# Kernel tuning notes

Hardware: AMD Instinct MI355X
Metric: run time of the kernel (lower is better)

The kernel has to match this reference:

```python
import jax, jax.numpy as jnp
import numpy as np

MAX_REL = 7  # maxRelativeDist

def _rel_pos_table(L, max_rel):
    # |i-j|, with distances beyond max_rel mapped to max_rel + log2(d - max_rel), clipped to [0, 2*max_rel]
    idx = jnp.arange(L)
    d = jnp.abs(idx[:, None] - idx[None, :]).astype(jnp.float32)
    far = d > max_rel
    d = jnp.where(far, max_rel + jnp.log2(jnp.maximum(d - max_rel, 1.0)), d)
    return jnp.clip(d, 0, 2 * max_rel).astype(jnp.int32)  # [L, L]

def setup_inputs() -> dict:
    key = jax.random.key(0)
    ks = jax.random.split(key, 16)
    B, L, C, P, H, DK = 8, 2048, 512, 64, 8, 64
    s = 0.02
    inp = {
        'qx': jax.random.normal(ks[0], (B, L, C), jnp.float32),
        'kx': jax.random.normal(ks[1], (B, L, C), jnp.float32),
        'vx': jax.random.normal(ks[2], (B, L, C), jnp.float32),
        'maskPAD': jnp.ones((B, L, L), jnp.int32),
        # pseudoAttn: Linear(C, P)
        'Wp': jax.random.normal(ks[3], (C, P), jnp.float32) * s,
        'bp': jnp.zeros((P,), jnp.float32),
        # WQ/WK: Linear(C, dkEnhance*DK*H) with dkEnhance=1
        'Wq': jax.random.normal(ks[4], (C, H * DK), jnp.float32) * s,
        'bq': jnp.zeros((H * DK,), jnp.float32),
        'Wk': jax.random.normal(ks[5], (C, H * DK), jnp.float32) * s,
        'bk': jnp.zeros((H * DK,), jnp.float32),
        'Wv': jax.random.normal(ks[6], (C, H * DK), jnp.float32) * s,
        'bv': jnp.zeros((H * DK,), jnp.float32),
        'Wo': jax.random.normal(ks[7], (H * DK, C), jnp.float32) * s,
        'bo': jnp.zeros((C,), jnp.float32),
        # relative position embeddings: [2*MAX_REL+1, H]
        'embK': jax.random.normal(ks[8], (2 * MAX_REL + 1, H), jnp.float32) * s,
        'embB': jax.random.normal(ks[9], (2 * MAX_REL + 1, H), jnp.float32) * s,
    }
    return inp

def reference(qx, kx, vx, maskPAD, Wp, bp, Wq, bq, Wk, bk, Wv, bv, Wo, bo, embK, embB):
    # dropout is identity (eval mode); preScores=None
    B, L, C = qx.shape
    H = embK.shape[1]
    DK = Wv.shape[1] // H
    P = Wp.shape[1]

    # pseudo-token compression
    pScore = vx @ Wp + bp                                   # [B, L, P]
    mask = (maskPAD[:, 0] == 0)[:, :, None]                 # [B, L, 1]
    pScore = jnp.where(mask, jnp.float32(-2.0 ** 15), pScore)
    pAlpha = jax.nn.softmax(pScore, axis=1)                 # softmax over L
    kxc = jnp.einsum('blp,blc->bpc', pAlpha, kx)            # [B, P, C]
    vxc = jnp.einsum('blp,blc->bpc', pAlpha, vx)            # [B, P, C]
    pAlpha_d = jax.lax.stop_gradient(pAlpha)

    # multi-head projections
    q = (qx @ Wq + bq).reshape(B, L, H, DK)                 # [B, L, H, DK]
    k = (kxc @ Wk + bk).reshape(B, P, H, DK)
    v = (vxc @ Wv + bv).reshape(B, P, H, DK)

    scores = jnp.einsum('blhd,bphd->bhlp', q, k) / np.sqrt(DK)  # [B, H, L, P]

    # relative-position modulation
    relTab = _rel_pos_table(L, MAX_REL)                     # [L, L] int
    Kmat = jnp.transpose(embK[relTab], (2, 1, 0))           # [H, L, L]
    Bmat = jnp.transpose(embB[relTab], (2, 1, 0))           # [H, L, L]
    Kterm = jnp.einsum('hlm,bmp->bhlp', Kmat, pAlpha_d)
    Bterm = jnp.einsum('hlm,bmp->bhlp', Bmat, pAlpha_d)
    scores = scores * Kterm + Bterm

    alpha = jax.nn.softmax(scores, axis=3)                  # over pseudo tokens
    z = jnp.einsum('bhlp,bphd->blhd', alpha, v).reshape(B, L, H * DK)
    z = z @ Wo + bo                                         # [B, L, C]
    return z, pScore, scores
```

## Files before the change

kernel.cpp:

```cpp
#include <hip/hip_runtime.h>


typedef __attribute__((ext_vector_type(8))) short bhalf8;
typedef __attribute__((ext_vector_type(4))) float fx4;

__device__ __forceinline__ unsigned short f2bf(float f) {
  union { float f; unsigned u; } v; v.f = f;
  unsigned u = v.u + 0x7fffu + ((v.u >> 16) & 1u);
  return (unsigned short)(u >> 16);
}
__device__ __forceinline__ float bf2f(unsigned short h) {
  union { unsigned u; float f; } v; v.u = ((unsigned)h) << 16;
  return v.f;
}
__device__ __forceinline__ void gld16(const void* g, void* l) {
  __builtin_amdgcn_global_load_lds(
      (const __attribute__((address_space(1))) void*)g,
      (__attribute__((address_space(3))) void*)l, 16, 0, 0);
}

template <int BM, int BN, int CMODE, int AF32, int KSPLIT, int BF32>
__device__ __forceinline__ void gemm_body(
    int bxx, int byy, int bzz, char* smemc,
    const void* __restrict__ Av, const unsigned short* __restrict__ BT,
    const float* __restrict__ bias, void* __restrict__ Cout,
    int K, int lda, int ldbt, int ldc, int HDIV,
    long sAb, long sAh, long sBb, long sBh, long sCb, long sCh, long sCk,
    const int* __restrict__ mpad, float* __restrict__ aux,
    const float* __restrict__ Bf32)
{
  constexpr int NA = BM / 16, NB = BN / 16, NT = NA + NB;
  constexpr int WM = BM / 2, WN = BN / 2, FM = WM / 16, FN = WN / 16;
  unsigned short* lds = (unsigned short*)smemc;
  const int t = threadIdx.x, l = t & 63, w = t >> 6;
  const int wr = w >> 1, wc = w & 1;
  const int zz = bzz, b = zz / HDIV, h = zz % HDIV;
  const int row0 = KSPLIT ? 0 : byy * BM;
  const int koff = KSPLIT ? byy * K : 0;
  const long cko = KSPLIT ? (long)byy * sCk : 0;
  const int col0 = bxx * BN;
  const unsigned short* Ag = (const unsigned short*)Av + b * sAb + h * sAh + (long)row0 * lda + koff;
  const float* AgF = (const float*)Av + b * sAb + h * sAh + (long)row0 * lda + koff;
  const unsigned short* Bg = BT + b * sBb + h * sBh + (long)col0 * ldbt + koff;
  const int lr = l & 15, lc = l >> 4;

  fx4 acc[FM][FN];
#pragma unroll
  for (int i = 0; i < FM; ++i)
#pragma unroll
    for (int j = 0; j < FN; ++j) acc[i][j] = fx4{0.f, 0.f, 0.f, 0.f};

  for (int k0 = 0; k0 < K; k0 += 32) {
#pragma unroll
    for (int i = 0; i < NT / 4; ++i) {
      const int tile = w + i * 4;
      bool handled = false;
      if constexpr (AF32 == 1) {
        if (tile < NA) {
          const float* gf = AgF + (long)(tile * 16 + lr) * lda + k0 + lc * 8;
          float4 x = *(const float4*)gf, y = *(const float4*)(gf + 4);
          bhalf8 pk;
          pk[0] = (short)f2bf(x.x); pk[1] = (short)f2bf(x.y);
          pk[2] = (short)f2bf(x.z); pk[3] = (short)f2bf(x.w);
          pk[4] = (short)f2bf(y.x); pk[5] = (short)f2bf(y.y);
          pk[6] = (short)f2bf(y.z); pk[7] = (short)f2bf(y.w);
          *(bhalf8*)&lds[tile * 512 + l * 8] = pk;
          handled = true;
        }
      } else if constexpr (AF32 == 2) {
        if (tile < NA) {
          const float* gf = (const float*)Av + (long)zz * sAb + (long)byy * 131072
                            + (long)(tile * 16 + lr) * 512 + k0 + lc * 8;
          float4 x = make_float4(0.f, 0.f, 0.f, 0.f), y = x;
#pragma unroll
          for (int c = 0; c < 4; ++c) {
            float4 a = *(const float4*)(gf + (long)c * 32768);
            float4 bq = *(const float4*)(gf + (long)c * 32768 + 4);
            x.x += a.x; x.y += a.y; x.z += a.z; x.w += a.w;
            y.x += bq.x; y.y += bq.y; y.z += bq.z; y.w += bq.w;
          }
          bhalf8 pk;
          pk[0] = (short)f2bf(x.x); pk[1] = (short)f2bf(x.y);
          pk[2] = (short)f2bf(x.z); pk[3] = (short)f2bf(x.w);
          pk[4] = (short)f2bf(y.x); pk[5] = (short)f2bf(y.y);
          pk[6] = (short)f2bf(y.z); pk[7] = (short)f2bf(y.w);
          *(bhalf8*)&lds[tile * 512 + l * 8] = pk;
          handled = true;
        }
      }
      if (!handled) {
        if constexpr (BF32 == 1) {
          const int ct = tile - NA;
          const float* gfB = Bf32 + (long)(k0 + lc * 8) * ldbt + col0 + ct * 16 + lr;
          bhalf8 pk;
#pragma unroll
          for (int i2 = 0; i2 < 8; ++i2) pk[i2] = (short)f2bf(gfB[(long)i2 * ldbt]);
          *(bhalf8*)&lds[tile * 512 + l * 8] = pk;
        } else {
          const unsigned short* g = (tile < NA)
              ? Ag + (long)(tile * 16 + lr) * lda + k0 + lc * 8
              : Bg + (long)((tile - NA) * 16 + lr) * ldbt + k0 + lc * 8;
          gld16(g, &lds[tile * 512]);
        }
      }
    }
    __syncthreads();
    bhalf8 af[FM], bf[FN];
#pragma unroll
    for (int i = 0; i < FM; ++i) af[i] = *(const bhalf8*)&lds[(wr * FM + i) * 512 + l * 8];
#pragma unroll
    for (int j = 0; j < FN; ++j) bf[j] = *(const bhalf8*)&lds[(NA + wc * FN + j) * 512 + l * 8];
#pragma unroll
    for (int i = 0; i < FM; ++i)
#pragma unroll
      for (int j = 0; j < FN; ++j)
        acc[i][j] = __builtin_amdgcn_mfma_f32_16x16x32_bf16(af[i], bf[j], acc[i][j], 0, 0, 0);
    __syncthreads();
  }

  if constexpr (CMODE == 3) {
    float (*tbuf)[65] = (float(*)[65])(smemc + NT * 1024);
#pragma unroll
    for (int fm = 0; fm < FM; ++fm) {
#pragma unroll
      for (int fn = 0; fn < FN; ++fn) {
        const int rg0 = row0 + wr * WM + fm * 16 + lc * 4;
        const int cg = col0 + wc * WN + fn * 16 + lr;
        const float bb = bias[cg];
#pragma unroll
        for (int jj = 0; jj < 4; ++jj) {
          const int rg = rg0 + jj;
          float vv = acc[fm][fn][jj] + bb;
          if (mpad[((long)(rg >> 11)) * (2048L * 2048) + (rg & 2047)] == 0) vv = -32768.f;
          __builtin_nontemporal_store(vv, (float*)Cout + (long)rg * ldc + cg);
          tbuf[rg - row0][cg] = vv;
        }
      }
    }
    __syncthreads();
    const int b0 = row0 >> 11, l0b = row0 & 2047;
    const int pp = t >> 2, li0 = (t & 3) * 16;
    float* dst = aux + ((long)b0 * 64 + pp) * 2048 + l0b + li0;
#pragma unroll
    for (int i = 0; i < 16; i += 4) {
      float4 o = make_float4(tbuf[li0 + i][pp],     tbuf[li0 + i + 1][pp],
                             tbuf[li0 + i + 2][pp], tbuf[li0 + i + 3][pp]);
      *(float4*)(dst + i) = o;
    }
  } else {
#pragma unroll
    for (int fm = 0; fm < FM; ++fm) {
#pragma unroll
      for (int fn = 0; fn < FN; ++fn) {
        const int rg0 = row0 + wr * WM + fm * 16 + lc * 4;
        const int cg = col0 + wc * WN + fn * 16 + lr;
        float bb = 0.f;
        if constexpr (CMODE == 4) {
          bb = (zz == 0) ? bias[cg] : ((const float*)mpad)[cg];
        } else {
          bb = bias ? bias[cg] : 0.f;
        }
#pragma unroll
        for (int jj = 0; jj < 4; ++jj) {
          const int rg = rg0 + jj;
          const float v = acc[fm][fn][jj] + bb;
          if constexpr (CMODE == 0) {
            ((float*)Cout)[b * sCb + h * sCh + cko + (long)rg * ldc + cg] = v;
          } else if constexpr (CMODE == 1) {
            ((unsigned short*)Cout)[b * sCb + h * sCh + (long)rg * ldc + cg] = f2bf(v);
          } else if constexpr (CMODE == 2) {
            ((unsigned short*)Cout)[(((long)(rg >> 6) * 8 + (cg >> 6)) * 64 + (cg & 63)) * 64 + (rg & 63)] = f2bf(v);
          } else if constexpr (CMODE == 4) {
            if (zz == 0)
              ((unsigned short*)Cout)[(long)rg * ldc + cg] = f2bf(v);
            else
              ((unsigned short*)Cout)[262144 + (((long)(rg >> 6) * 8 + (cg >> 6)) * 64 + (cg & 63)) * 64 + (rg & 63)] = f2bf(v);
          } else {
            __builtin_nontemporal_store(v, (float*)Cout + b * sCb + h * sCh + cko + (long)rg * ldc + cg);
          }
        }
      }
    }
  }
}

template <int BM, int BN, int CMODE, int AF32, int KSPLIT>
__global__ __launch_bounds__(256)
void gemm_mfma(const void* __restrict__ Av, const unsigned short* __restrict__ BT,
               const float* __restrict__ bias, void* __restrict__ Cout,
               int K, int lda, int ldbt, int ldc, int HDIV,
               long sAb, long sAh, long sBb, long sBh, long sCb, long sCh, long sCk,
               const int* __restrict__ mpad, float* __restrict__ aux)
{
  constexpr int SM = (BM / 16 + BN / 16) * 1024 + (CMODE == 3 ? 16640 : 0);
  __shared__ __align__(16) char smem[SM];
  gemm_body<BM, BN, CMODE, AF32, KSPLIT, 0>(blockIdx.x, blockIdx.y, blockIdx.z, smem,
      Av, BT, bias, Cout, K, lda, ldbt, ldc, HDIV,
      sAb, sAh, sBb, sBh, sCb, sCh, sCk, mpad, aux, nullptr);
}

__device__ __forceinline__ void tr_body(float (*tile)[65], const float* __restrict__ in,
                                        unsigned short* __restrict__ out,
                                        int R, int Cd, int r0, int c0, int t)
{
  const int tr = t >> 4, tc4 = (t & 15) * 4;
#pragma unroll
  for (int pass = 0; pass < 4; ++pass) {
    int r = pass * 16 + tr;
    float4 v = *(const float4*)(in + (long)(r0 + r) * Cd + c0 + tc4);
    tile[r][tc4] = v.x; tile[r][tc4 + 1] = v.y; tile[r][tc4 + 2] = v.z; tile[r][tc4 + 3] = v.w;
  }
  __syncthreads();
#pragma unroll
  for (int pass = 0; pass < 4; ++pass) {
    int c = pass * 16 + tr;
    ushort4 o;
    o.x = f2bf(tile[tc4][c]);     o.y = f2bf(tile[tc4 + 1][c]);
    o.z = f2bf(tile[tc4 + 2][c]); o.w = f2bf(tile[tc4 + 3][c]);
    *(ushort4*)(out + (long)(c0 + c) * R + r0 + tc4) = o;
  }
}

__global__ __launch_bounds__(256)
void combo0(const float* __restrict__ vx, const float* __restrict__ Wp,
            const float* __restrict__ bp, const int* __restrict__ maskPAD,
            float* __restrict__ ps_out, float* __restrict__ pScoreT,
            const float* __restrict__ kx,
            const float* __restrict__ Wq, const float* __restrict__ Wk,
            const float* __restrict__ Wv, const float* __restrict__ Wo,
            unsigned short* __restrict__ kxT, unsigned short* __restrict__ vxT,
            unsigned short* __restrict__ WqT, unsigned short* __restrict__ WkT,
            unsigned short* __restrict__ WvT, unsigned short* __restrict__ WoT)
{
  __shared__ __align__(16) char smem[24832];
  const int id = blockIdx.x;
  const long LC = 2048L * 512;
  if (id < 256) {
    gemm_body<64, 64, 3, 1, 0, 1>(0, id, 0, smem,
        vx, nullptr, bp, ps_out, 512, 512, 64, 64, 1,
        0, 0, 0, 0, 0, 0, 0, maskPAD, pScoreT, Wp);
  } else if (id < 4352) {
    const int r = id - 256;
    const int zz = r >> 8, rem = r & 255;
    const float* in = (zz < 8) ? kx + zz * LC : vx + (zz - 8) * LC;
    unsigned short* out = (zz < 8) ? kxT + zz * LC : vxT + (zz - 8) * LC;
    tr_body((float(*)[65])smem, in, out, 2048, 512, (rem >> 3) * 64, (rem & 7) * 64, threadIdx.x);
  } else if (id < 4608) {
    const int r = id - 4352;
    const int z = r >> 6, rem = r & 63;
    const float* in; unsigned short* out;
    switch (z) {
      case 0: in = Wq; out = WqT; break;
      case 1: in = Wk; out = WkT; break;
      case 2: in = Wv; out = WvT; break;
      default: in = Wo; out = WoT; break;
    }
    tr_body((float(*)[65])smem, in, out, 512, 512, (rem >> 3) * 64, (rem & 7) * 64, threadIdx.x);
  }
}

__device__ __forceinline__ void kb_body(int bx, int by, char* smemc,
    const unsigned short* __restrict__ PSb,
    const float* __restrict__ embK, const float* __restrict__ embB,
    ushort2* __restrict__ KB)
{
  const int L = 2048, STR = 338;
  unsigned short* psw = (unsigned short*)smemc;
  float (*eKs)[8] = (float(*)[8])(smemc + 43264);
  float (*eBs)[8] = (float(*)[8])(smemc + 43264 + 512);
  const int t = threadIdx.x, b = by, l0 = bx * 64;
  if (t < 128) {
    int r = t >> 3, h = t & 7;
    eKs[r][h] = (r < 15) ? embK[r * 8 + h] : 0.f;
    eBs[r][h] = (r < 15) ? embB[r * 8 + h] : 0.f;
  }
  const int W0 = l0 - 136;
  const int w = t >> 6, ln = t & 63;
  for (int pr = w * 16; pr < w * 16 + 16; ++pr) {
    const unsigned short* src = PSb + ((long)b * 64 + pr) * 2048;
#pragma unroll
    for (int pass = 0; pass < 6; ++pass) {
      int j = pass * 64 + ln;
      if (j < 337) {
        int g = (j == 336) ? (L - 1) : (W0 + j);
        g = g < 0 ? 0 : (g > L - 1 ? L - 1 : g);
        psw[pr * STR + j] = src[g];
      }
    }
  }
  __syncthreads();
  const int p = ln;
  const int Btab[14] = {0,1,2,3,4,5,6,8,10,14,22,38,70,134};
  for (int step = 0; step < 16; ++step) {
    const int l = l0 + w * 16 + step;
    float U[15];
#pragma unroll
    for (int r = 0; r < 14; ++r) {
      int hi = l + Btab[r]; hi = hi > L - 1 ? L - 1 : hi;
      float u = bf2f(psw[p * STR + (hi - W0)]);
      const int lo = l - 1 - Btab[r];
      if (lo >= 0) u -= bf2f(psw[p * STR + (lo - W0)]);
      U[r] = u;
    }
    U[14] = bf2f(psw[p * STR + 336]);
    for (int h = 0; h < 8; ++h) {
      float Kt = 0.f, Bt = 0.f;
#pragma unroll
      for (int r = 0; r < 15; ++r) {
        Kt = fmaf(eKs[r][h] - eKs[r + 1][h], U[r], Kt);
        Bt = fmaf(eBs[r][h] - eBs[r + 1][h], U[r], Bt);
      }
      ushort2 o; o.x = f2bf(Kt); o.y = f2bf(Bt);
      KB[(((long)(b * 8 + h)) * L + l) * 64 + p] = o;
    }
  }
}

__global__ __launch_bounds__(256)
void combo1(const unsigned short* __restrict__ pAbf, const unsigned short* __restrict__ kxT,
            float* __restrict__ pbuf,
            const unsigned short* __restrict__ PSb,
            const float* __restrict__ embK, const float* __restrict__ embB,
            ushort2* __restrict__ KB)
{
  __shared__ __align__(16) char smem[44544];
  const int id = blockIdx.x;
  if (id < 512) {
    gemm_body<64, 64, 0, 0, 1, 0>(id & 7, (id >> 3) & 3, id >> 5, smem,
        pAbf, kxT, nullptr, pbuf, 512, 2048, 2048, 512, 2,
        131072, 0, 1048576, 8388608, 131072, 1048576, 32768, nullptr, nullptr, nullptr);
  } else {
    const int r = id - 512;
    kb_body(r & 31, r >> 5, smem, PSb, embK, embB, KB);
  }
}

__global__ __launch_bounds__(256)
void combo2(const float* __restrict__ pbuf, const unsigned short* __restrict__ WkT,
            const float* __restrict__ bk, const float* __restrict__ bv,
            unsigned short* __restrict__ kp,
            const float* __restrict__ qx, const unsigned short* __restrict__ WqT,
            const float* __restrict__ bq, unsigned short* __restrict__ qbf)
{
  __shared__ __align__(16) char smem[16384];
  const int id = blockIdx.x;
  if (id < 64) {
    gemm_body<64, 128, 4, 2, 0, 0>(id & 3, (id >> 2) & 7, id >> 5, smem,
        pbuf, WkT, bk, kp, 512, 512, 512, 512, 1,
        1048576, 0, 262144, 0, 0, 0, 0, (const int*)bv, nullptr, nullptr);
  } else {
    const int r = id - 64;
    gemm_body<128, 128, 1, 1, 0, 0>(r & 3, r >> 2, 0, smem,
        qx, WqT, bq, qbf, 512, 512, 512, 512, 1,
        0, 0, 0, 0, 0, 0, 0, nullptr, nullptr, nullptr);
  }
}

__global__ __launch_bounds__(256)
void softmax_scan(const float* __restrict__ pScoreT,
                  unsigned short* __restrict__ PSb, unsigned short* __restrict__ pA_bf)
{
  __shared__ float red[256];
  const int p = blockIdx.x, b = blockIdx.y, t = threadIdx.x;
  const float* row = pScoreT + ((size_t)b * 64 + p) * 2048;
  float4 va = ((const float4*)row)[t * 2], vb = ((const float4*)row)[t * 2 + 1];
  float v[8] = {va.x, va.y, va.z, va.w, vb.x, vb.y, vb.z, vb.w};
  float mx = v[0];
#pragma unroll
  for (int i = 1; i < 8; ++i) mx = fmaxf(mx, v[i]);
  red[t] = mx; __syncthreads();
  for (int s = 128; s > 0; s >>= 1) { if (t < s) red[t] = fmaxf(red[t], red[t + s]); __syncthreads(); }
  float m = red[0]; __syncthreads();
  float e[8]; float s = 0.f;
#pragma unroll
  for (int i = 0; i < 8; ++i) { e[i] = expf(v[i] - m); s += e[i]; }
  red[t] = s; __syncthreads();
  for (int o = 1; o < 256; o <<= 1) {
    float x = (t >= o) ? red[t - o] : 0.f;
    __syncthreads(); red[t] += x; __syncthreads();
  }
  float inv = 1.0f / red[255];
  float run = red[t] - s;
  size_t base = ((size_t)b * 64 + p) * 2048 + (size_t)t * 8;
#pragma unroll
  for (int i = 0; i < 8; ++i) {
    run += e[i];
    PSb[base + i] = f2bf(run * inv);
    pA_bf[base + i] = f2bf(e[i] * inv);
  }
}

__global__ __launch_bounds__(256)
void attn_fused(const unsigned short* __restrict__ qb,
                const unsigned short* __restrict__ kp,
                const unsigned short* __restrict__ vpT,
                const ushort2* __restrict__ KB,
                float* __restrict__ sc_out,
                unsigned short* __restrict__ zpre)
{
  const int L = 2048;
  __shared__ __align__(16) unsigned short stg[24 * 512];
  unsigned short* qkb = &stg[8 * 512];
  const int t = threadIdx.x, l = t & 63, w = t >> 6, lr = l & 15, lc = l >> 4;
  const int flat = blockIdx.y * 16 + blockIdx.x;
  const int swz = (flat & 7) * 128 + (flat >> 3);
  const int z = swz >> 4, b = z >> 3, h = z & 7;
  const int l0 = (swz & 15) * 128;
  const unsigned short* Ag = qb + ((long)(b * L + l0)) * 512 + h * 64;
  const unsigned short* Bg = kp + (long)b * 64 * 512 + h * 64;
#pragma unroll
  for (int i = 0; i < 6; ++i) {
    const int tile = w + i * 4;
    const unsigned short* g;
    if (tile < 16) { int rt = tile >> 1, ks = tile & 1; g = Ag + (long)(rt * 16 + lr) * 512 + ks * 32 + lc * 8; }
    else { int j = tile - 16; int rt = j >> 1, ks = j & 1; g = Bg + (long)(rt * 16 + lr) * 512 + ks * 32 + lc * 8; }
    gld16(g, &stg[tile * 512]);
  }
  const ushort2* kbb = KB + (((long)(b * 8 + h)) * L + l0) * 64 + l;
  unsigned int kbreg[32];
#pragma unroll
  for (int i = 0; i < 32; ++i)
    kbreg[i] = *(const unsigned int*)(kbb + ((long)(w * 32 + i)) * 64);
  __syncthreads();
  const int wr = w >> 1, wc = w & 1;
  fx4 acc[4][2];
#pragma unroll
  for (int i = 0; i < 4; ++i)
#pragma unroll
    for (int j = 0; j < 2; ++j) acc[i][j] = fx4{0.f, 0.f, 0.f, 0.f};
#pragma unroll
  for (int ks = 0; ks < 2; ++ks) {
    bhalf8 af[4], bf[2];
#pragma unroll
    for (int i = 0; i < 4; ++i) af[i] = *(const bhalf8*)&stg[((wr * 4 + i) * 2 + ks) * 512 + l * 8];
#pragma unroll
    for (int j = 0; j < 2; ++j) bf[j] = *(const bhalf8*)&stg[(16 + (wc * 2 + j) * 2 + ks) * 512 + l * 8];
#pragma unroll
    for (int i = 0; i < 4; ++i)
#pragma unroll
      for (int j = 0; j < 2; ++j)
        acc[i][j] = __builtin_amdgcn_mfma_f32_16x16x32_bf16(af[i], bf[j], acc[i][j], 0, 0, 0);
  }
  __syncthreads();
#pragma unroll
  for (int fm = 0; fm < 4; ++fm)
#pragma unroll
    for (int fn = 0; fn < 2; ++fn)
#pragma unroll
      for (int jj = 0; jj < 4; ++jj) {
        const int row = wr * 64 + fm * 16 + lc * 4 + jj;
        const int col = wc * 32 + fn * 16 + lr;
        *(unsigned short*)((char*)qkb + ((row * 128 + col * 2) ^ ((row & 7) << 4))) = f2bf(acc[fm][fn][jj]);
      }
  __syncthreads();
  {
    const unsigned short* Vg = vpT + ((long)(b * 8 + h)) * 64 * 64;
#pragma unroll
    for (int i = 0; i < 2; ++i) {
      const int tile = w + i * 4, rt = tile >> 1, ks = tile & 1;
      gld16(Vg + (long)(rt * 16 + lr) * 64 + ks * 32 + lc * 8, &stg[tile * 512]);
    }
  }
  const int p = l;
  float* scb = sc_out + ((long)(b * 8 + h) * L + l0) * 64 + p;
#pragma unroll
  for (int c = 0; c < 8; ++c) {
    const int rbase = w * 32 + c * 4;
    float sv[4];
#pragma unroll
    for (int il = 0; il < 4; ++il) {
      const int row = rbase + il;
      const unsigned int kbw = kbreg[c * 4 + il];
      const float qkv = bf2f(*(const unsigned short*)((const char*)qkb + ((row * 128 + p * 2) ^ ((row & 7) << 4))));
      sv[il] = qkv * 0.125f * bf2f((unsigned short)(kbw & 0xffffu)) + bf2f((unsigned short)(kbw >> 16));
      __builtin_nontemporal_store(sv[il], scb + (long)row * 64);
    }
    float mx[4] = {sv[0], sv[1], sv[2], sv[3]};
#pragma unroll
    for (int o = 32; o > 0; o >>= 1)
#pragma unroll
      for (int il = 0; il < 4; ++il) mx[il] = fmaxf(mx[il], __shfl_xor(mx[il], o, 64));
    float ex[4], sm[4];
#pragma unroll
    for (int il = 0; il < 4; ++il) { ex[il] = __expf(sv[il] - mx[il]); sm[il] = ex[il]; }
#pragma unroll
    for (int o = 32; o > 0; o >>= 1)
#pragma unroll
      for (int il = 0; il < 4; ++il) sm[il] += __shfl_xor(sm[il], o, 64);
#pragma unroll
    for (int il = 0; il < 4; ++il) {
      const int row = rbase + il;
      *(unsigned short*)((char*)qkb + ((row * 128 + p * 2) ^ ((row & 7) << 4))) = f2bf(ex[il] / sm[il]);
    }
  }
  __syncthreads();
  fx4 a2[4][2];
#pragma unroll
  for (int i = 0; i < 4; ++i)
#pragma unroll
    for (int j = 0; j < 2; ++j) a2[i][j] = fx4{0.f, 0.f, 0.f, 0.f};
#pragma unroll
  for (int ks = 0; ks < 2; ++ks) {
    bhalf8 paf[4], pvf[2];
#pragma unroll
    for (int i = 0; i < 4; ++i) {
      const int row = (wr * 4 + i) * 16 + lr;
      paf[i] = *(const bhalf8*)((const char*)qkb + ((row * 128 + ks * 64 + lc * 16) ^ ((row & 7) << 4)));
    }
#pragma unroll
    for (int j = 0; j < 2; ++j)
      pvf[j] = *(const bhalf8*)&stg[(((wc * 2 + j) * 2 + ks) * 512) + l * 8];
#pragma unroll
    for (int i = 0; i < 4; ++i)
#pragma unroll
      for (int j = 0; j < 2; ++j)
        a2[i][j] = __builtin_amdgcn_mfma_f32_16x16x32_bf16(paf[i], pvf[j], a2[i][j], 0, 0, 0);
  }
#pragma unroll
  for (int fm = 0; fm < 4; ++fm)
#pragma unroll
    for (int fn = 0; fn < 2; ++fn)
#pragma unroll
      for (int jj = 0; jj < 4; ++jj) {
        const int row = wr * 64 + fm * 16 + lc * 4 + jj;
        const int col = wc * 32 + fn * 16 + lr;
        zpre[((long)(b * L + l0 + row)) * 512 + h * 64 + col] = f2bf(a2[fm][fn][jj]);
      }
}

extern "C" void kernel_launch(void* const* d_in, const int* in_sizes, int n_in,
                              void* d_out, int out_size, void* d_ws, size_t ws_size,
                              hipStream_t stream)
{
  const int B = 8, L = 2048, C = 512, P = 64;
  const float* qx = (const float*)d_in[0];
  const float* kx = (const float*)d_in[1];
  const float* vx = (const float*)d_in[2];
  const int* maskPAD = (const int*)d_in[3];
  const float* Wp = (const float*)d_in[4];
  const float* bp = (const float*)d_in[5];
  const float* Wq = (const float*)d_in[6];
  const float* bq = (const float*)d_in[7];
  const float* Wk = (const float*)d_in[8];
  const float* bk = (const float*)d_in[9];
  const float* Wv = (const float*)d_in[10];
  const float* bv = (const float*)d_in[11];
  const float* Wo = (const float*)d_in[12];
  const float* bo = (const float*)d_in[13];
  const float* embK = (const float*)d_in[14];
  const float* embB = (const float*)d_in[15];

  float* z_out  = (float*)d_out;
  float* ps_out = z_out + (size_t)B * L * C;
  float* sc_out = ps_out + (size_t)B * L * P;

  char* w8 = (char*)d_ws;
  size_t o = 0;
  auto take = [&](size_t n) { char* r = w8 + o; o += n; return r; };
  unsigned short* R_A  = (unsigned short*)take(16777216);
  unsigned short* R_B  = (unsigned short*)take(16777216);
  unsigned short* kxT  = (unsigned short*)take(16777216);
  unsigned short* vxT  = (unsigned short*)take(16777216);
  unsigned short* WqT  = (unsigned short*)take(524288);
  unsigned short* WkT  = (unsigned short*)take(524288);
  unsigned short* WvT  = (unsigned short*)take(524288);
  unsigned short* WoT  = (unsigned short*)take(524288);
  float* pScoreT       = (float*)take(4194304);
  unsigned short* PSb  = (unsigned short*)take(2097152);
  unsigned short* pAbf = (unsigned short*)take(2097152);
  float* pbuf          = (float*)take(8388608);
  unsigned short* kp   = (unsigned short*)take(1048576);
  ushort2* KB          = (ushort2*)take(33554432);

  combo0<<<dim3(4616), 256, 0, stream>>>(
      vx, Wp, bp, maskPAD, ps_out, pScoreT, kx,
      Wq, Wk, Wv, Wo, kxT, vxT, WqT, WkT, WvT, WoT);
  softmax_scan<<<dim3(P, B), 256, 0, stream>>>(pScoreT, PSb, pAbf);
  combo1<<<dim3(768), 256, 0, stream>>>(pAbf, kxT, pbuf, PSb, embK, embB, KB);
  combo2<<<dim3(576), 256, 0, stream>>>(pbuf, WkT, bk, bv, kp, qx, WqT, bq, R_B);
  attn_fused<<<dim3(16, 64), 256, 0, stream>>>(
      R_B, kp, kp + 262144, KB, sc_out, R_A);
  gemm_mfma<128, 128, 5, 0, 0><<<dim3(4, 128, 1), 256, 0, stream>>>(
      R_A, WoT, bo, z_out, 512, 512, 512, 512, 1, 0, 0, 0, 0, 0, 0, 0, nullptr, nullptr);
}
```

Baseline: 200.9 us.

## Read kx/vx fp32 directly in compression GEMM, drop bf16 transpose pass

Removes the combo0 stage that transposed and converted kx and vx into bf16 kxT/vxT buffers. The pAlpha-weighted compression GEMM in combo1 now loads B tiles straight from the fp32 kx/vx inputs with strided scalar reads, converting to bf16 on the fly and picking kx or vx by head index. This avoids writing and re-reading two 16 MB intermediates and shrinks combo0's grid. In exchange the GEMM's B loads become uncoalesced strided scalar loads, replacing the async global-to-LDS copy.

```diff
diff --git a/kernel.cpp b/kernel.cpp
--- a/kernel.cpp
+++ b/kernel.cpp
@@ -27,7 +27,7 @@
     int K, int lda, int ldbt, int ldc, int HDIV,
     long sAb, long sAh, long sBb, long sBh, long sCb, long sCh, long sCk,
     const int* __restrict__ mpad, float* __restrict__ aux,
-    const float* __restrict__ Bf32)
+    const float* __restrict__ Bf32, const float* __restrict__ Bf32b)
 {
   constexpr int NA = BM / 16, NB = BN / 16, NT = NA + NB;
   constexpr int WM = BM / 2, WN = BN / 2, FM = WM / 16, FN = WN / 16;
@@ -54,9 +54,8 @@
 #pragma unroll
     for (int i = 0; i < NT / 4; ++i) {
       const int tile = w + i * 4;
-      bool handled = false;
-      if constexpr (AF32 == 1) {
-        if (tile < NA) {
+      if (tile < NA) {
+        if constexpr (AF32 == 1) {
           const float* gf = AgF + (long)(tile * 16 + lr) * lda + k0 + lc * 8;
           float4 x = *(const float4*)gf, y = *(const float4*)(gf + 4);
           bhalf8 pk;
@@ -65,10 +64,7 @@
           pk[4] = (short)f2bf(y.x); pk[5] = (short)f2bf(y.y);
           pk[6] = (short)f2bf(y.z); pk[7] = (short)f2bf(y.w);
           *(bhalf8*)&lds[tile * 512 + l * 8] = pk;
-          handled = true;
-        }
-      } else if constexpr (AF32 == 2) {
-        if (tile < NA) {
+        } else if constexpr (AF32 == 2) {
           const float* gf = (const float*)Av + (long)zz * sAb + (long)byy * 131072
                             + (long)(tile * 16 + lr) * 512 + k0 + lc * 8;
           float4 x = make_float4(0.f, 0.f, 0.f, 0.f), y = x;
@@ -85,22 +81,27 @@
           pk[4] = (short)f2bf(y.x); pk[5] = (short)f2bf(y.y);
           pk[6] = (short)f2bf(y.z); pk[7] = (short)f2bf(y.w);
           *(bhalf8*)&lds[tile * 512 + l * 8] = pk;
-          handled = true;
+        } else {
+          gld16(Ag + (long)(tile * 16 + lr) * lda + k0 + lc * 8, &lds[tile * 512]);
         }
-      }
-      if (!handled) {
+      } else {
         if constexpr (BF32 == 1) {
           const int ct = tile - NA;
-          const float* gfB = Bf32 + (long)(k0 + lc * 8) * ldbt + col0 + ct * 16 + lr;
+          const float* gfB = Bf32 + (long)(koff + k0 + lc * 8) * ldbt + col0 + ct * 16 + lr;
           bhalf8 pk;
 #pragma unroll
           for (int i2 = 0; i2 < 8; ++i2) pk[i2] = (short)f2bf(gfB[(long)i2 * ldbt]);
           *(bhalf8*)&lds[tile * 512 + l * 8] = pk;
+        } else if constexpr (BF32 == 2) {
+          const int ct = tile - NA;
+          const float* src = (h ? Bf32b : Bf32) + (long)b * 1048576
+                             + (long)(koff + k0 + lc * 8) * ldbt + col0 + ct * 16 + lr;
+          bhalf8 pk;
+#pragma unroll
+          for (int i2 = 0; i2 < 8; ++i2) pk[i2] = (short)f2bf(src[(long)i2 * ldbt]);
+          *(bhalf8*)&lds[tile * 512 + l * 8] = pk;
         } else {
-          const unsigned short* g = (tile < NA)
-              ? Ag + (long)(tile * 16 + lr) * lda + k0 + lc * 8
-              : Bg + (long)((tile - NA) * 16 + lr) * ldbt + k0 + lc * 8;
-          gld16(g, &lds[tile * 512]);
+          gld16(Bg + (long)((tile - NA) * 16 + lr) * ldbt + k0 + lc * 8, &lds[tile * 512]);
         }
       }
     }
@@ -196,7 +197,7 @@
   __shared__ __align__(16) char smem[SM];
   gemm_body<BM, BN, CMODE, AF32, KSPLIT, 0>(blockIdx.x, blockIdx.y, blockIdx.z, smem,
       Av, BT, bias, Cout, K, lda, ldbt, ldc, HDIV,
-      sAb, sAh, sBb, sBh, sCb, sCh, sCk, mpad, aux, nullptr);
+      sAb, sAh, sBb, sBh, sCb, sCh, sCk, mpad, aux, nullptr, nullptr);
 }
 
 __device__ __forceinline__ void tr_body(float (*tile)[65], const float* __restrict__ in,
@@ -225,28 +226,19 @@
 void combo0(const float* __restrict__ vx, const float* __restrict__ Wp,
             const float* __restrict__ bp, const int* __restrict__ maskPAD,
             float* __restrict__ ps_out, float* __restrict__ pScoreT,
-            const float* __restrict__ kx,
             const float* __restrict__ Wq, const float* __restrict__ Wk,
             const float* __restrict__ Wv, const float* __restrict__ Wo,
-            unsigned short* __restrict__ kxT, unsigned short* __restrict__ vxT,
             unsigned short* __restrict__ WqT, unsigned short* __restrict__ WkT,
             unsigned short* __restrict__ WvT, unsigned short* __restrict__ WoT)
 {
   __shared__ __align__(16) char smem[24832];
   const int id = blockIdx.x;
-  const long LC = 2048L * 512;
   if (id < 256) {
     gemm_body<64, 64, 3, 1, 0, 1>(0, id, 0, smem,
         vx, nullptr, bp, ps_out, 512, 512, 64, 64, 1,
-        0, 0, 0, 0, 0, 0, 0, maskPAD, pScoreT, Wp);
-  } else if (id < 4352) {
+        0, 0, 0, 0, 0, 0, 0, maskPAD, pScoreT, Wp, nullptr);
+  } else {
     const int r = id - 256;
-    const int zz = r >> 8, rem = r & 255;
-    const float* in = (zz < 8) ? kx + zz * LC : vx + (zz - 8) * LC;
-    unsigned short* out = (zz < 8) ? kxT + zz * LC : vxT + (zz - 8) * LC;
-    tr_body((float(*)[65])smem, in, out, 2048, 512, (rem >> 3) * 64, (rem & 7) * 64, threadIdx.x);
-  } else if (id < 4608) {
-    const int r = id - 4352;
     const int z = r >> 6, rem = r & 63;
     const float* in; unsigned short* out;
     switch (z) {
@@ -317,7 +309,8 @@
 }
 
 __global__ __launch_bounds__(256)
-void combo1(const unsigned short* __restrict__ pAbf, const unsigned short* __restrict__ kxT,
+void combo1(const unsigned short* __restrict__ pAbf,
+            const float* __restrict__ kx, const float* __restrict__ vx,
             float* __restrict__ pbuf,
             const unsigned short* __restrict__ PSb,
             const float* __restrict__ embK, const float* __restrict__ embB,
@@ -326,9 +319,9 @@
   __shared__ __align__(16) char smem[44544];
   const int id = blockIdx.x;
   if (id < 512) {
-    gemm_body<64, 64, 0, 0, 1, 0>(id & 7, (id >> 3) & 3, id >> 5, smem,
-        pAbf, kxT, nullptr, pbuf, 512, 2048, 2048, 512, 2,
-        131072, 0, 1048576, 8388608, 131072, 1048576, 32768, nullptr, nullptr, nullptr);
+    gemm_body<64, 64, 0, 0, 1, 2>(id & 7, (id >> 3) & 3, id >> 5, smem,
+        pAbf, nullptr, nullptr, pbuf, 512, 2048, 512, 512, 2,
+        131072, 0, 0, 0, 131072, 1048576, 32768, nullptr, nullptr, kx, vx);
   } else {
     const int r = id - 512;
     kb_body(r & 31, r >> 5, smem, PSb, embK, embB, KB);
@@ -347,12 +340,12 @@
   if (id < 64) {
     gemm_body<64, 128, 4, 2, 0, 0>(id & 3, (id >> 2) & 7, id >> 5, smem,
         pbuf, WkT, bk, kp, 512, 512, 512, 512, 1,
-        1048576, 0, 262144, 0, 0, 0, 0, (const int*)bv, nullptr, nullptr);
+        1048576, 0, 262144, 0, 0, 0, 0, (const int*)bv, nullptr, nullptr, nullptr);
   } else {
     const int r = id - 64;
     gemm_body<128, 128, 1, 1, 0, 0>(r & 3, r >> 2, 0, smem,
         qx, WqT, bq, qbf, 512, 512, 512, 512, 1,
-        0, 0, 0, 0, 0, 0, 0, nullptr, nullptr, nullptr);
+        0, 0, 0, 0, 0, 0, 0, nullptr, nullptr, nullptr, nullptr);
   }
 }
 
@@ -559,8 +552,6 @@
   auto take = [&](size_t n) { char* r = w8 + o; o += n; return r; };
   unsigned short* R_A  = (unsigned short*)take(16777216);
   unsigned short* R_B  = (unsigned short*)take(16777216);
-  unsigned short* kxT  = (unsigned short*)take(16777216);
-  unsigned short* vxT  = (unsigned short*)take(16777216);
   unsigned short* WqT  = (unsigned short*)take(524288);
   unsigned short* WkT  = (unsigned short*)take(524288);
   unsigned short* WvT  = (unsigned short*)take(524288);
@@ -572,11 +563,11 @@
   unsigned short* kp   = (unsigned short*)take(1048576);
   ushort2* KB          = (ushort2*)take(33554432);
 
-  combo0<<<dim3(4616), 256, 0, stream>>>(
-      vx, Wp, bp, maskPAD, ps_out, pScoreT, kx,
-      Wq, Wk, Wv, Wo, kxT, vxT, WqT, WkT, WvT, WoT);
+  combo0<<<dim3(512), 256, 0, stream>>>(
+      vx, Wp, bp, maskPAD, ps_out, pScoreT,
+      Wq, Wk, Wv, Wo, WqT, WkT, WvT, WoT);
   softmax_scan<<<dim3(P, B), 256, 0, stream>>>(pScoreT, PSb, pAbf);
-  combo1<<<dim3(768), 256, 0, stream>>>(pAbf, kxT, pbuf, PSb, embK, embB, KB);
+  combo1<<<dim3(768), 256, 0, stream>>>(pAbf, kx, vx, pbuf, PSb, embK, embB, KB);
   combo2<<<dim3(576), 256, 0, stream>>>(pbuf, WkT, bk, bv, kp, qx, WqT, bq, R_B);
   attn_fused<<<dim3(16, 64), 256, 0, stream>>>(
       R_B, kp, kp + 262144, KB, sc_out, R_A);
```

After: 198.3 us (median of 3 runs). About the same (-1.3%).
